# Performance work log

Measured on AMD Instinct MI355X. Metric: run time of the kernel, lower is better.

The kernel has to match this reference:

```python
import jax, jax.numpy as jnp
import numpy as np

FEATURES_DIM = 64 * (64 * 10 + 1)  # 41024


def setup_inputs() -> dict:
    key = jax.random.key(0)
    ks = jax.random.split(key, 11)
    def lin(k, out_d, in_d):
        bound = 1.0 / np.sqrt(in_d)
        kw, kb = jax.random.split(k)
        W = jax.random.uniform(kw, (out_d, in_d), jnp.float32, -bound, bound)
        b = jax.random.uniform(kb, (out_d,), jnp.float32, -bound, bound)
        return W, b
    x = jax.random.uniform(ks[0], (2 * FEATURES_DIM,), jnp.float32)
    W_my, b_my = lin(ks[1], 256, FEATURES_DIM)
    W_opp, b_opp = lin(ks[2], 256, FEATURES_DIM)
    W1, b1 = lin(ks[3], 32, 512)
    W2, b2 = lin(ks[4], 32, 32)
    W3, b3 = lin(ks[5], 1, 32)
    return {"x": x, "W_my": W_my, "b_my": b_my, "W_opp": W_opp, "b_opp": b_opp,
            "W1": W1, "b1": b1, "W2": W2, "b2": b2, "W3": W3, "b3": b3}


def reference(x, W_my, b_my, W_opp, b_opp, W1, b1, W2, b2, W3, b3):
    # HalfKP accumulators: two huge sparse-linear (here dense) 41024->256 + ReLU
    my = jax.nn.relu(W_my @ x[:FEATURES_DIM] + b_my)      # [256]
    opp = jax.nn.relu(W_opp @ x[FEATURES_DIM:] + b_opp)   # [256]
    h = jnp.concatenate([my, opp])                        # [512]
    # small trailing MLP 512->32->32->1
    h = jax.nn.relu(W1 @ h + b1)
    h = jax.nn.relu(W2 @ h + b2)
    return W3 @ h + b3                                    # [1]
```

## Files before the change

kernel.cpp:

```cpp
#include <hip/hip_runtime.h>

#define FEAT 41024
#define NF4  (FEAT / 4)

__global__ __launch_bounds__(256) void halfkp_matvec(
    const float* __restrict__ x,
    const float* __restrict__ W_my,  const float* __restrict__ b_my,
    const float* __restrict__ W_opp, const float* __restrict__ b_opp,
    float* __restrict__ h)
{
    const int row = blockIdx.x;
    const int tid = threadIdx.x;

    const float4* __restrict__ W4 =
        (const float4*)(row < 256 ? W_my : W_opp) + (size_t)(row & 255) * NF4;
    const float4* __restrict__ x4 =
        (const float4*)x + (row < 256 ? 0 : NF4);
    const float bias = (row < 256) ? b_my[row] : b_opp[row - 256];

    float a0 = 0.f, a1 = 0.f, a2 = 0.f, a3 = 0.f;
    int i = tid;
    #pragma unroll
    for (int k = 0; k < 10; ++k) {
        float4 w0 = W4[i      ]; float4 v0 = x4[i      ];
        float4 w1 = W4[i + 256]; float4 v1 = x4[i + 256];
        float4 w2 = W4[i + 512]; float4 v2 = x4[i + 512];
        float4 w3 = W4[i + 768]; float4 v3 = x4[i + 768];
        a0 += w0.x*v0.x + w0.y*v0.y + w0.z*v0.z + w0.w*v0.w;
        a1 += w1.x*v1.x + w1.y*v1.y + w1.z*v1.z + w1.w*v1.w;
        a2 += w2.x*v2.x + w2.y*v2.y + w2.z*v2.z + w2.w*v2.w;
        a3 += w3.x*v3.x + w3.y*v3.y + w3.z*v3.z + w3.w*v3.w;
        i += 1024;
    }
    if (tid < 16) {
        float4 w = W4[10240 + tid]; float4 v = x4[10240 + tid];
        a0 += w.x*v.x + w.y*v.y + w.z*v.z + w.w*v.w;
    }

    float acc = (a0 + a1) + (a2 + a3);
    #pragma unroll
    for (int off = 32; off > 0; off >>= 1)
        acc += __shfl_down(acc, off, 64);

    __shared__ float red[4];
    if ((tid & 63) == 0) red[tid >> 6] = acc;
    __syncthreads();

    if (tid == 0) {
        float s = red[0] + red[1] + red[2] + red[3] + bias;
        h[row] = s > 0.f ? s : 0.f;
    }
}

__global__ __launch_bounds__(256) void mlp_head(
    const float* __restrict__ h,
    const float* __restrict__ W1, const float* __restrict__ b1,
    const float* __restrict__ W2, const float* __restrict__ b2,
    const float* __restrict__ W3, const float* __restrict__ b3,
    float* __restrict__ out)
{
    __shared__ float hs[512];
    __shared__ float h1[32];
    __shared__ float h2[32];

    const int tid = threadIdx.x;
    hs[tid]       = h[tid];
    hs[tid + 256] = h[tid + 256];
    __syncthreads();

    const int o = tid >> 3;
    const int j = tid & 7;
    float acc = 0.f;
    const float* __restrict__ w = W1 + o * 512 + j * 64;
    #pragma unroll 8
    for (int k = 0; k < 64; ++k)
        acc += w[k] * hs[j * 64 + k];
    acc += __shfl_down(acc, 4, 64);
    acc += __shfl_down(acc, 2, 64);
    acc += __shfl_down(acc, 1, 64);
    if (j == 0) {
        float s = acc + b1[o];
        h1[o] = s > 0.f ? s : 0.f;
    }
    __syncthreads();

    if (tid < 32) {
        float s = b2[tid];
        #pragma unroll 8
        for (int k = 0; k < 32; ++k)
            s += W2[tid * 32 + k] * h1[k];
        h2[tid] = s > 0.f ? s : 0.f;
    }
    __syncthreads();

    if (tid == 0) {
        float s = b3[0];
        #pragma unroll 8
        for (int k = 0; k < 32; ++k)
            s += W3[k] * h2[k];
        out[0] = s;
    }
}

extern "C" void kernel_launch(void* const* d_in, const int* in_sizes, int n_in,
                              void* d_out, int out_size, void* d_ws, size_t ws_size,
                              hipStream_t stream)
{
    const float* x     = (const float*)d_in[0];
    const float* W_my  = (const float*)d_in[1];
    const float* b_my  = (const float*)d_in[2];
    const float* W_opp = (const float*)d_in[3];
    const float* b_opp = (const float*)d_in[4];
    const float* W1    = (const float*)d_in[5];
    const float* b1    = (const float*)d_in[6];
    const float* W2    = (const float*)d_in[7];
    const float* b2    = (const float*)d_in[8];
    const float* W3    = (const float*)d_in[9];
    const float* b3    = (const float*)d_in[10];

    float* out = (float*)d_out;
    float* h   = (float*)d_ws;

    halfkp_matvec<<<512, 256, 0, stream>>>(x, W_my, b_my, W_opp, b_opp, h);
    mlp_head<<<1, 256, 0, stream>>>(h, W1, b1, W2, b2, W3, b3, out);
}
```

Baseline: 23.99 us.

## Split each accumulator row across two blocks and widen MLP head

```diff
diff --git a/kernel.cpp b/kernel.cpp
--- a/kernel.cpp
+++ b/kernel.cpp
@@ -1,27 +1,31 @@
 #include <hip/hip_runtime.h>
 
-#define FEAT 41024
-#define NF4  (FEAT / 4)
+#define FEAT  41024
+#define NF4   (FEAT / 4)
+#define HALF4 (NF4 / 2)
+#define NBLK  1024
 
-__global__ __launch_bounds__(256) void halfkp_matvec(
+__global__ __launch_bounds__(256) void halfkp_matvec_part(
     const float* __restrict__ x,
-    const float* __restrict__ W_my,  const float* __restrict__ b_my,
-    const float* __restrict__ W_opp, const float* __restrict__ b_opp,
-    float* __restrict__ h)
+    const float* __restrict__ W_my,
+    const float* __restrict__ W_opp,
+    float* __restrict__ partial)
 {
-    const int row = blockIdx.x;
-    const int tid = threadIdx.x;
+    const int b    = blockIdx.x;
+    const int tid  = threadIdx.x;
+    const int row  = b >> 1;
+    const int half = b & 1;
 
     const float4* __restrict__ W4 =
-        (const float4*)(row < 256 ? W_my : W_opp) + (size_t)(row & 255) * NF4;
+        (const float4*)(row < 256 ? W_my : W_opp)
+        + (size_t)(row & 255) * NF4 + (size_t)half * HALF4;
     const float4* __restrict__ x4 =
-        (const float4*)x + (row < 256 ? 0 : NF4);
-    const float bias = (row < 256) ? b_my[row] : b_opp[row - 256];
+        (const float4*)x + (row < 256 ? 0 : NF4) + (size_t)half * HALF4;
 
     float a0 = 0.f, a1 = 0.f, a2 = 0.f, a3 = 0.f;
     int i = tid;
     #pragma unroll
-    for (int k = 0; k < 10; ++k) {
+    for (int k = 0; k < 5; ++k) {
         float4 w0 = W4[i      ]; float4 v0 = x4[i      ];
         float4 w1 = W4[i + 256]; float4 v1 = x4[i + 256];
         float4 w2 = W4[i + 512]; float4 v2 = x4[i + 512];
@@ -32,8 +36,8 @@
         a3 += w3.x*v3.x + w3.y*v3.y + w3.z*v3.z + w3.w*v3.w;
         i += 1024;
     }
-    if (tid < 16) {
-        float4 w = W4[10240 + tid]; float4 v = x4[10240 + tid];
+    if (tid < 8) {
+        float4 w = W4[5120 + tid]; float4 v = x4[5120 + tid];
         a0 += w.x*v.x + w.y*v.y + w.z*v.z + w.w*v.w;
     }
 
@@ -45,18 +49,16 @@
     __shared__ float red[4];
     if ((tid & 63) == 0) red[tid >> 6] = acc;
     __syncthreads();
-
-    if (tid == 0) {
-        float s = red[0] + red[1] + red[2] + red[3] + bias;
-        h[row] = s > 0.f ? s : 0.f;
-    }
+    if (tid == 0)
+        partial[b] = red[0] + red[1] + red[2] + red[3];
 }
 
-__global__ __launch_bounds__(256) void mlp_head(
-    const float* __restrict__ h,
-    const float* __restrict__ W1, const float* __restrict__ b1,
-    const float* __restrict__ W2, const float* __restrict__ b2,
-    const float* __restrict__ W3, const float* __restrict__ b3,
+__global__ __launch_bounds__(1024) void mlp_head(
+    const float* __restrict__ partial,
+    const float* __restrict__ b_my, const float* __restrict__ b_opp,
+    const float* __restrict__ W1,  const float* __restrict__ b1,
+    const float* __restrict__ W2,  const float* __restrict__ b2,
+    const float* __restrict__ W3,  const float* __restrict__ b3,
     float* __restrict__ out)
 {
     __shared__ float hs[512];
@@ -64,20 +66,32 @@
     __shared__ float h2[32];
 
     const int tid = threadIdx.x;
-    hs[tid]       = h[tid];
-    hs[tid + 256] = h[tid + 256];
+    const int o = tid >> 5;
+    const int j = tid & 31;
+
+    float w[16];
+    #pragma unroll
+    for (int k = 0; k < 16; ++k)
+        w[k] = W1[o * 512 + j + 32 * k];
+
+    if (tid < 512) {
+        float p0 = partial[2 * tid];
+        float p1 = partial[2 * tid + 1];
+        float bias = (tid < 256) ? b_my[tid] : b_opp[tid - 256];
+        float s = p0 + p1 + bias;
+        hs[tid] = s > 0.f ? s : 0.f;
+    }
     __syncthreads();
 
-    const int o = tid >> 3;
-    const int j = tid & 7;
     float acc = 0.f;
-    const float* __restrict__ w = W1 + o * 512 + j * 64;
-    #pragma unroll 8
-    for (int k = 0; k < 64; ++k)
-        acc += w[k] * hs[j * 64 + k];
-    acc += __shfl_down(acc, 4, 64);
-    acc += __shfl_down(acc, 2, 64);
-    acc += __shfl_down(acc, 1, 64);
+    #pragma unroll
+    for (int k = 0; k < 16; ++k)
+        acc += w[k] * hs[j + 32 * k];
+    acc += __shfl_down(acc, 16, 32);
+    acc += __shfl_down(acc,  8, 32);
+    acc += __shfl_down(acc,  4, 32);
+    acc += __shfl_down(acc,  2, 32);
+    acc += __shfl_down(acc,  1, 32);
     if (j == 0) {
         float s = acc + b1[o];
         h1[o] = s > 0.f ? s : 0.f;
@@ -118,9 +132,10 @@
     const float* W3    = (const float*)d_in[9];
     const float* b3    = (const float*)d_in[10];
 
-    float* out = (float*)d_out;
-    float* h   = (float*)d_ws;
+    float* out     = (float*)d_out;
+    float* partial = (float*)d_ws;
 
-    halfkp_matvec<<<512, 256, 0, stream>>>(x, W_my, b_my, W_opp, b_opp, h);
-    mlp_head<<<1, 256, 0, stream>>>(h, W1, b1, W2, b2, W3, b3, out);
+    halfkp_matvec_part<<<NBLK, 256, 0, stream>>>(x, W_my, W_opp, partial);
+    mlp_head<<<1, 1024, 0, stream>>>(partial, b_my, b_opp,
+                                     W1, b1, W2, b2, W3, b3, out);
 }
```

After: 22.42 us. 1.07x faster.

## Fuse first MLP layer into matvec via binned atomics and widen blocks

Applied to the files above, without the earlier changes.

```diff
diff --git a/kernel.cpp b/kernel.cpp
--- a/kernel.cpp
+++ b/kernel.cpp
@@ -1,13 +1,16 @@
 #include <hip/hip_runtime.h>
 
-#define FEAT 41024
-#define NF4  (FEAT / 4)
+#define FEAT  41024
+#define NF4   (FEAT / 4)
+#define NROWS 512
+#define NBINS 8
 
-__global__ __launch_bounds__(256) void halfkp_matvec(
+__global__ __launch_bounds__(512) void halfkp_matvec_l1(
     const float* __restrict__ x,
     const float* __restrict__ W_my,  const float* __restrict__ b_my,
     const float* __restrict__ W_opp, const float* __restrict__ b_opp,
-    float* __restrict__ h)
+    const float* __restrict__ W1,
+    float* __restrict__ bins)
 {
     const int row = blockIdx.x;
     const int tid = threadIdx.x;
@@ -16,21 +19,20 @@
         (const float4*)(row < 256 ? W_my : W_opp) + (size_t)(row & 255) * NF4;
     const float4* __restrict__ x4 =
         (const float4*)x + (row < 256 ? 0 : NF4);
-    const float bias = (row < 256) ? b_my[row] : b_opp[row - 256];
 
     float a0 = 0.f, a1 = 0.f, a2 = 0.f, a3 = 0.f;
     int i = tid;
     #pragma unroll
-    for (int k = 0; k < 10; ++k) {
-        float4 w0 = W4[i      ]; float4 v0 = x4[i      ];
-        float4 w1 = W4[i + 256]; float4 v1 = x4[i + 256];
-        float4 w2 = W4[i + 512]; float4 v2 = x4[i + 512];
-        float4 w3 = W4[i + 768]; float4 v3 = x4[i + 768];
+    for (int k = 0; k < 5; ++k) {
+        float4 w0 = W4[i       ]; float4 v0 = x4[i       ];
+        float4 w1 = W4[i +  512]; float4 v1 = x4[i +  512];
+        float4 w2 = W4[i + 1024]; float4 v2 = x4[i + 1024];
+        float4 w3 = W4[i + 1536]; float4 v3 = x4[i + 1536];
         a0 += w0.x*v0.x + w0.y*v0.y + w0.z*v0.z + w0.w*v0.w;
         a1 += w1.x*v1.x + w1.y*v1.y + w1.z*v1.z + w1.w*v1.w;
         a2 += w2.x*v2.x + w2.y*v2.y + w2.z*v2.z + w2.w*v2.w;
         a3 += w3.x*v3.x + w3.y*v3.y + w3.z*v3.z + w3.w*v3.w;
-        i += 1024;
+        i += 2048;
     }
     if (tid < 16) {
         float4 w = W4[10240 + tid]; float4 v = x4[10240 + tid];
@@ -42,58 +44,55 @@
     for (int off = 32; off > 0; off >>= 1)
         acc += __shfl_down(acc, off, 64);
 
-    __shared__ float red[4];
+    __shared__ float red[8];
     if ((tid & 63) == 0) red[tid >> 6] = acc;
     __syncthreads();
 
+    __shared__ float hval;
     if (tid == 0) {
-        float s = red[0] + red[1] + red[2] + red[3] + bias;
-        h[row] = s > 0.f ? s : 0.f;
+        float s = red[0] + red[1] + red[2] + red[3]
+                + red[4] + red[5] + red[6] + red[7]
+                + ((row < 256) ? b_my[row] : b_opp[row - 256]);
+        hval = s > 0.f ? s : 0.f;
+    }
+    __syncthreads();
+
+    if (tid < 32) {
+        float v = hval * W1[tid * 512 + row];
+        atomicAdd(&bins[(row & (NBINS - 1)) * 32 + tid], v);
     }
 }
 
-__global__ __launch_bounds__(256) void mlp_head(
-    const float* __restrict__ h,
-    const float* __restrict__ W1, const float* __restrict__ b1,
+__global__ __launch_bounds__(64) void mlp_tail(
+    const float* __restrict__ bins,
+    const float* __restrict__ b1,
     const float* __restrict__ W2, const float* __restrict__ b2,
     const float* __restrict__ W3, const float* __restrict__ b3,
     float* __restrict__ out)
 {
-    __shared__ float hs[512];
     __shared__ float h1[32];
     __shared__ float h2[32];
+    const int t = threadIdx.x;
 
-    const int tid = threadIdx.x;
-    hs[tid]       = h[tid];
-    hs[tid + 256] = h[tid + 256];
-    __syncthreads();
-
-    const int o = tid >> 3;
-    const int j = tid & 7;
-    float acc = 0.f;
-    const float* __restrict__ w = W1 + o * 512 + j * 64;
-    #pragma unroll 8
-    for (int k = 0; k < 64; ++k)
-        acc += w[k] * hs[j * 64 + k];
-    acc += __shfl_down(acc, 4, 64);
-    acc += __shfl_down(acc, 2, 64);
-    acc += __shfl_down(acc, 1, 64);
-    if (j == 0) {
-        float s = acc + b1[o];
-        h1[o] = s > 0.f ? s : 0.f;
+    if (t < 32) {
+        float s = b1[t];
+        #pragma unroll
+        for (int g = 0; g < NBINS; ++g)
+            s += bins[g * 32 + t];
+        h1[t] = s > 0.f ? s : 0.f;
     }
     __syncthreads();
 
-    if (tid < 32) {
-        float s = b2[tid];
+    if (t < 32) {
+        float s = b2[t];
         #pragma unroll 8
         for (int k = 0; k < 32; ++k)
-            s += W2[tid * 32 + k] * h1[k];
-        h2[tid] = s > 0.f ? s : 0.f;
+            s += W2[t * 32 + k] * h1[k];
+        h2[t] = s > 0.f ? s : 0.f;
     }
     __syncthreads();
 
-    if (tid == 0) {
+    if (t == 0) {
         float s = b3[0];
         #pragma unroll 8
         for (int k = 0; k < 32; ++k)
@@ -118,9 +117,11 @@
     const float* W3    = (const float*)d_in[9];
     const float* b3    = (const float*)d_in[10];
 
-    float* out = (float*)d_out;
-    float* h   = (float*)d_ws;
+    float* out  = (float*)d_out;
+    float* bins = (float*)d_ws;
 
-    halfkp_matvec<<<512, 256, 0, stream>>>(x, W_my, b_my, W_opp, b_opp, h);
-    mlp_head<<<1, 256, 0, stream>>>(h, W1, b1, W2, b2, W3, b3, out);
+    hipMemsetAsync(bins, 0, NBINS * 32 * sizeof(float), stream);
+    halfkp_matvec_l1<<<NROWS, 512, 0, stream>>>(x, W_my, b_my, W_opp, b_opp,
+                                                W1, bins);
+    mlp_tail<<<1, 64, 0, stream>>>(bins, b1, W2, b2, W3, b3, out);
 }
```

Result: slower. 27.94 us (+16.5%).
